# Kernel tuning notes

Measured on AMD Instinct MI355X. Metric: run time of the kernel, lower is better.

The kernel has to match this reference:

```python
import jax, jax.numpy as jnp
import numpy as np

D_MODEL = 1024
N_HEADS = 16
MAX_SEQ = 1024
BATCH = 4

def _first_primes(n):
    limit = n * 15
    sieve = np.ones(limit, dtype=bool)
    sieve[:2] = False
    for i in range(2, int(limit ** 0.5) + 1):
        if sieve[i]:
            sieve[i * i::i] = False
    return np.flatnonzero(sieve)[:n]

def _pi_attention_bias(n_heads, max_seq_len):
    # bias[h, t, s] = 0.1 * sin(prime[h]*pi * (t - s) / max_seq_len)
    primes = _first_primes(n_heads).astype(np.float32)
    freqs = primes * np.pi  # [H]
    pos = np.arange(max_seq_len, dtype=np.float32)
    pos_diff = pos[:, None] - pos[None, :]  # [T, T]
    bias = np.sin(freqs[:, None, None] * pos_diff[None] / max_seq_len) * 0.1
    return jnp.asarray(bias, dtype=jnp.float32)

def setup_inputs() -> dict:
    key = jax.random.key(0)
    ks = jax.random.split(key, 8)
    D = D_MODEL
    xavier = (6.0 / (D + D)) ** 0.5
    inp = {
        'x': jax.random.normal(ks[0], (BATCH, MAX_SEQ, D), dtype=jnp.float32),
        'Wq': jax.random.uniform(ks[1], (D, D), jnp.float32, -xavier, xavier),
        'bq': jnp.zeros((D,), jnp.float32),
        'Wk': jax.random.uniform(ks[2], (D, D), jnp.float32, -xavier, xavier),
        'bk': jnp.zeros((D,), jnp.float32),
        'Wv': jax.random.uniform(ks[3], (D, D), jnp.float32, -xavier, xavier),
        'bv': jnp.zeros((D,), jnp.float32),
        'Wo': jax.random.uniform(ks[4], (D, D), jnp.float32, -xavier, xavier),
        'bo': jnp.zeros((D,), jnp.float32),
        'pi_bias': _pi_attention_bias(N_HEADS, MAX_SEQ),
        'bias_scale': jnp.asarray(0.1, jnp.float32),
        'spectral_alpha': jnp.asarray(1.0, jnp.float32),
    }
    return inp

def reference(x, Wq, bq, Wk, bk, Wv, bv, Wo, bo, pi_bias, bias_scale, spectral_alpha):
    B, T, D = x.shape
    H = N_HEADS
    hd = D // H
    scale = 1.0 / (hd ** 0.5)

    def split_heads(y):
        return y.reshape(B, T, H, hd).transpose(0, 2, 1, 3)  # [B,H,T,hd]

    q = split_heads(x @ Wq + bq)
    k = split_heads(x @ Wk + bk)
    v = split_heads(x @ Wv + bv)

    # spectral filter along the time axis (use_spectral and T > 4)
    freqs = jnp.fft.fftfreq(T).astype(jnp.float32)  # [T]
    filt = jnp.exp(-jnp.abs(spectral_alpha) * jnp.abs(freqs))[None, None, :, None]
    q = jnp.fft.ifft(jnp.fft.fft(q, axis=2, norm='ortho') * filt, axis=2, norm='ortho').real
    k = jnp.fft.ifft(jnp.fft.fft(k, axis=2, norm='ortho') * filt, axis=2, norm='ortho').real

    scores = jnp.einsum('bhtd,bhsd->bhts', q, k) * scale
    scores = scores + bias_scale * pi_bias[None, :, :T, :T]
    attn = jax.nn.softmax(scores, axis=-1)  # dropout is identity in eval
    out = jnp.einsum('bhts,bhsd->bhtd', attn, v)
    out = out.transpose(0, 2, 1, 3).reshape(B, T, D)
    return out @ Wo + bo
```

## Files before the change

kernel.cpp:

```cpp
#include <hip/hip_runtime.h>
#include <hip/hip_bf16.h>

typedef __bf16 bf16x8 __attribute__((ext_vector_type(8)));
typedef float f32x4 __attribute__((ext_vector_type(4)));

#define OFF_GMAT   0x10000ULL
#define OFF_XB     0x210000ULL
#define OFF_XBT    0xA10000ULL
#define OFF_XF     0x1210000ULL
#define OFF_WQT    0x1A10000ULL
#define OFF_WKT    0x1C10000ULL
#define OFF_WVT    0x1E10000ULL
#define OFF_WOT    0x2010000ULL
#define OFF_KB     0x2210000ULL
#define OFF_VTB    0x2A10000ULL

static __device__ __forceinline__ unsigned short f2bf(float f) {
  union { float f; unsigned int u; } v; v.f = f;
  unsigned int r = v.u + 0x7FFFu + ((v.u >> 16) & 1u);
  return (unsigned short)(r >> 16);
}

static __device__ __forceinline__ void g2l16(const unsigned short* g, unsigned short* l) {
  __builtin_amdgcn_global_load_lds(
      (const __attribute__((address_space(1))) unsigned int*)g,
      (__attribute__((address_space(3))) unsigned int*)l, 16, 0, 0);
}

__constant__ float PRIMES_F[16] = {2.f, 3.f, 5.f, 7.f, 11.f, 13.f, 17.f, 19.f,
                                   23.f, 29.f, 31.f, 37.f, 41.f, 43.f, 47.f, 53.f};

__global__ __launch_bounds__(256) void k_prep(
    const float* __restrict__ x, const float* __restrict__ w0,
    const float* __restrict__ w1, const float* __restrict__ w2,
    const float* __restrict__ w3, const float* __restrict__ alpha_p,
    unsigned short* __restrict__ xb, unsigned short* __restrict__ xbT,
    unsigned short* __restrict__ Wout, unsigned short* __restrict__ Gm) {
  __shared__ float tile[32][33];
  const int z = blockIdx.z;
  const int r0 = blockIdx.y * 32, c0 = blockIdx.x * 32;
  const int tx = threadIdx.x & 31, ty = threadIdx.x >> 5;
  if (z == 8) {
    const float alpha = fmaxf(fabsf(alpha_p[0]), 1e-6f);
    const float q = __expf(-alpha * (1.f / 1024.f));
    const float q512 = __expf(-alpha * 0.5f);
    #pragma unroll
    for (int i = 0; i < 4; i++) {
      const int t = r0 + ty + 8 * i, s = c0 + tx;
      const int d = (t - s) & 1023;
      float s_, c_;
      __sincosf((float)d * (6.28318530717958647692f / 1024.f), &s_, &c_);
      const float sgn = (d & 1) ? -1.f : 1.f;
      const float Nr = q * c_ - q512 * sgn, Ni = q * s_;
      const float Wr = 1.f - q * c_, Wi = -q * s_;
      const float sum = (Nr * Wr + Ni * Wi) / (Wr * Wr + Wi * Wi);
      const float gd = (1.f + q512 * sgn + 2.f * sum) * (1.f / 1024.f);
      Gm[(long)t * 1024 + s] = f2bf(gd);
    }
    return;
  }
  const bool isX = z < 4;
  const float* in = isX ? (x + ((long)z << 20))
                        : (z == 4 ? w0 : z == 5 ? w1 : z == 6 ? w2 : w3);
  const long ooff = isX ? ((long)z << 20) : ((long)(z - 4) << 20);
  #pragma unroll
  for (int i = 0; i < 4; i++) {
    float v = in[(long)(r0 + ty + 8 * i) * 1024 + c0 + tx];
    tile[ty + 8 * i][tx] = v;
    if (isX) xb[ooff + (long)(r0 + ty + 8 * i) * 1024 + c0 + tx] = f2bf(v);
  }
  __syncthreads();
  unsigned short* outT = isX ? xbT : Wout;
  #pragma unroll
  for (int i = 0; i < 4; i++)
    outT[ooff + (long)(c0 + ty + 8 * i) * 1024 + r0 + tx] = f2bf(tile[tx][ty + 8 * i]);
}

#define GEMM_CORE(A_, Bt_, ACC_)                                                     \
  const int tid = threadIdx.x, l = tid & 63, wid = tid >> 6;                         \
  const int lr = l & 15, lg = l >> 4;                                                \
  const int wm = (wid >> 1) * 64, wn = (wid & 1) * 64;                               \
  const int scol = ((l & 7) ^ (l >> 3)) * 8;                                         \
  const unsigned short* Ag = A_ + (long)(m0 + wid * 32 + (l >> 3)) * 1024 + scol;    \
  const unsigned short* Bg = Bt_ + (long)(n0 + wid * 32 + (l >> 3)) * 1024 + scol;   \
  const int xk = (lr & 7) << 4;                                                      \
  const int co[2] = {(0 + lg * 16) ^ xk, (64 + lg * 16) ^ xk};                       \
  {                                                                                  \
    _Pragma("unroll")                                                                \
    for (int c = 0; c < 4; c++) {                                                    \
      g2l16(Ag + (long)c * 8192, &As[0][wid * 2048 + c * 512]);                      \
      g2l16(Bg + (long)c * 8192, &Bs[0][wid * 2048 + c * 512]);                      \
    }                                                                                \
    Ag += 64; Bg += 64;                                                              \
  }                                                                                  \
  __syncthreads();                                                                   \
  for (int t = 0; t < 16; ++t) {                                                     \
    const int cur = t & 1;                                                           \
    if (t < 15) {                                                                    \
      const int nxt = cur ^ 1;                                                       \
      _Pragma("unroll")                                                              \
      for (int c = 0; c < 4; c++) {                                                  \
        g2l16(Ag + (long)c * 8192, &As[nxt][wid * 2048 + c * 512]);                  \
        g2l16(Bg + (long)c * 8192, &Bs[nxt][wid * 2048 + c * 512]);                  \
      }                                                                              \
      Ag += 64; Bg += 64;                                                            \
      asm volatile("s_waitcnt vmcnt(8)" ::: "memory");                               \
    } else {                                                                         \
      asm volatile("s_waitcnt vmcnt(0)" ::: "memory");                               \
    }                                                                                \
    __builtin_amdgcn_s_barrier();                                                    \
    __builtin_amdgcn_sched_barrier(0);                                               \
    const char* Ab = (const char*)&As[cur][0];                                       \
    const char* Bb = (const char*)&Bs[cur][0];                                       \
    _Pragma("unroll")                                                                \
    for (int ks = 0; ks < 2; ks++) {                                                 \
      bf16x8 af[4], bfr[4];                                                          \
      _Pragma("unroll")                                                              \
      for (int mf = 0; mf < 4; mf++)                                                 \
        af[mf] = *(const bf16x8*)(Ab + (wm + mf * 16 + lr) * 128 + co[ks]);          \
      _Pragma("unroll")                                                              \
      for (int nf = 0; nf < 4; nf++)                                                 \
        bfr[nf] = *(const bf16x8*)(Bb + (wn + nf * 16 + lr) * 128 + co[ks]);         \
      _Pragma("unroll")                                                              \
      for (int mf = 0; mf < 4; mf++)                                                 \
        _Pragma("unroll")                                                            \
        for (int nf = 0; nf < 4; nf++)                                               \
          ACC_[mf][nf] = __builtin_amdgcn_mfma_f32_16x16x32_bf16(af[mf], bfr[nf],    \
                                                                 ACC_[mf][nf], 0, 0, 0); \
    }                                                                                \
    __builtin_amdgcn_sched_barrier(0);                                               \
    __builtin_amdgcn_s_barrier();                                                    \
  }

__global__ __launch_bounds__(256) void k_gemm5(
    const unsigned short* __restrict__ A, const unsigned short* __restrict__ Bt,
    const float* __restrict__ bias, const float* __restrict__ bias2,
    unsigned short* __restrict__ Cv, unsigned short* __restrict__ Cv2) {
  __shared__ __align__(16) unsigned short As[2][128 * 64];
  __shared__ __align__(16) unsigned short Bs[2][128 * 64];
  const int orig = (blockIdx.x & 7) * 64 + (blockIdx.x >> 3);
  const int m0 = (orig & 31) * 128, n0 = (orig >> 5) * 128;
  f32x4 acc[4][4] = {};
  GEMM_CORE(A, Bt, acc)
  #pragma unroll
  for (int nf = 0; nf < 4; nf++) {
    const int n = n0 + wn + nf * 16 + lr;
    const float bb = (n < 1024) ? bias[n] : bias2[n - 1024];
    unsigned short* Cd = (n < 1024) ? Cv : Cv2;
    #pragma unroll
    for (int mf = 0; mf < 4; mf++) {
      const int mb = m0 + wm + mf * 16 + lg * 4;
      #pragma unroll
      for (int r = 0; r < 4; r++)
        Cd[(long)(mb + r) * 1024 + (n & 1023)] = f2bf(acc[mf][nf][r] + bb);
    }
  }
}

__global__ __launch_bounds__(256) void k_fv(
    const unsigned short* __restrict__ Gm, const unsigned short* __restrict__ xbT,
    const unsigned short* __restrict__ WvT, const unsigned short* __restrict__ xb,
    const float* __restrict__ bv, unsigned short* __restrict__ Xf,
    unsigned short* __restrict__ Vtb) {
  __shared__ __align__(16) unsigned short As[2][128 * 64];
  __shared__ __align__(16) unsigned short Bs[2][128 * 64];
  const bool isV = blockIdx.x < 256;
  const int inner = blockIdx.x & 255;
  const int o = (inner & 7) * 32 + (inner >> 3);
  const int m0 = (o & 7) * 128, n0 = (o >> 3) * 128;
  const unsigned short* A_ = isV ? WvT : Gm;
  const unsigned short* Bt_ = isV ? xb : xbT;
  const int nk = isV ? 16 : 6;
  const int ktbase = isV ? 0 : ((m0 - 128) & 1023);
  const int tid = threadIdx.x, l = tid & 63, wid = tid >> 6;
  const int lr = l & 15, lg = l >> 4;
  const int wm = (wid >> 1) * 64, wn = (wid & 1) * 64;
  const int scol = ((l & 7) ^ (l >> 3)) * 8;
  const unsigned short* Ag = A_ + (long)(m0 + wid * 32 + (l >> 3)) * 1024 + scol;
  const unsigned short* Bg = Bt_ + (long)(n0 + wid * 32 + (l >> 3)) * 1024 + scol;
  const int xk = (lr & 7) << 4;
  const int co[2] = {(0 + lg * 16) ^ xk, (64 + lg * 16) ^ xk};
  {
    #pragma unroll
    for (int c = 0; c < 4; c++) {
      g2l16(Ag + (long)c * 8192 + ktbase, &As[0][wid * 2048 + c * 512]);
      g2l16(Bg + (long)c * 8192 + ktbase, &Bs[0][wid * 2048 + c * 512]);
    }
  }
  __syncthreads();
  f32x4 acc[4][4] = {};
  for (int t = 0; t < nk; ++t) {
    const int cur = t & 1;
    if (t < nk - 1) {
      const int nxt = cur ^ 1;
      const int kt = (ktbase + ((t + 1) << 6)) & 1023;
      #pragma unroll
      for (int c = 0; c < 4; c++) {
        g2l16(Ag + (long)c * 8192 + kt, &As[nxt][wid * 2048 + c * 512]);
        g2l16(Bg + (long)c * 8192 + kt, &Bs[nxt][wid * 2048 + c * 512]);
      }
      asm volatile("s_waitcnt vmcnt(8)" ::: "memory");
    } else {
      asm volatile("s_waitcnt vmcnt(0)" ::: "memory");
    }
    __builtin_amdgcn_s_barrier();
    __builtin_amdgcn_sched_barrier(0);
    const char* Ab = (const char*)&As[cur][0];
    const char* Bb = (const char*)&Bs[cur][0];
    #pragma unroll
    for (int ks = 0; ks < 2; ks++) {
      bf16x8 af[4], bfr[4];
      #pragma unroll
      for (int mf = 0; mf < 4; mf++)
        af[mf] = *(const bf16x8*)(Ab + (wm + mf * 16 + lr) * 128 + co[ks]);
      #pragma unroll
      for (int nf = 0; nf < 4; nf++)
        bfr[nf] = *(const bf16x8*)(Bb + (wn + nf * 16 + lr) * 128 + co[ks]);
      #pragma unroll
      for (int mf = 0; mf < 4; mf++)
        #pragma unroll
        for (int nf = 0; nf < 4; nf++)
          acc[mf][nf] = __builtin_amdgcn_mfma_f32_16x16x32_bf16(af[mf], bfr[nf], acc[mf][nf], 0, 0, 0);
    }
    __builtin_amdgcn_sched_barrier(0);
    __builtin_amdgcn_s_barrier();
  }
  #pragma unroll
  for (int nf = 0; nf < 4; nf++) {
    const int n = n0 + wn + nf * 16 + lr;
    #pragma unroll
    for (int mf = 0; mf < 4; mf++) {
      const int mb = wm + mf * 16 + lg * 4;
      #pragma unroll
      for (int r = 0; r < 4; r++) {
        const int m = m0 + mb + r;
        float v = acc[mf][nf][r];
        if (isV) {
          Vtb[(long)m * 4096 + n] = f2bf(v + bv[m]);
        } else {
          Xf[(long)((n & ~1023) + m) * 1024 + (n & 1023)] = f2bf(v);
        }
      }
    }
  }
}

__global__ __launch_bounds__(256) void k_gemmO(
    const unsigned short* __restrict__ A, const unsigned short* __restrict__ Bt,
    const float* __restrict__ bias, float* __restrict__ C) {
  __shared__ __align__(16) unsigned short As[2][64 * 64];
  __shared__ __align__(16) unsigned short Bs[2][128 * 64];
  const int orig = (blockIdx.x & 7) * 64 + (blockIdx.x >> 3);
  const int m0 = (orig & 63) * 64, n0 = (orig >> 6) * 128;
  const int tid = threadIdx.x, l = tid & 63, wid = tid >> 6;
  const int lr = l & 15, lg = l >> 4;
  const int wm = (wid >> 1) * 32, wn = (wid & 1) * 64;
  const int scol = ((l & 7) ^ (l >> 3)) * 8;
  const unsigned short* Ag = A + (long)(m0 + wid * 16 + (l >> 3)) * 1024 + scol;
  const unsigned short* Bg = Bt + (long)(n0 + wid * 32 + (l >> 3)) * 1024 + scol;
  const int xk = (lr & 7) << 4;
  const int co[2] = {(0 + lg * 16) ^ xk, (64 + lg * 16) ^ xk};
  {
    #pragma unroll
    for (int c = 0; c < 2; c++) g2l16(Ag + (long)c * 8192, &As[0][wid * 1024 + c * 512]);
    #pragma unroll
    for (int c = 0; c < 4; c++) g2l16(Bg + (long)c * 8192, &Bs[0][wid * 2048 + c * 512]);
    Ag += 64; Bg += 64;
  }
  __syncthreads();
  f32x4 acc[2][4] = {};
  for (int t = 0; t < 16; ++t) {
    const int cur = t & 1;
    if (t < 15) {
      const int nxt = cur ^ 1;
      #pragma unroll
      for (int c = 0; c < 2; c++) g2l16(Ag + (long)c * 8192, &As[nxt][wid * 1024 + c * 512]);
      #pragma unroll
      for (int c = 0; c < 4; c++) g2l16(Bg + (long)c * 8192, &Bs[nxt][wid * 2048 + c * 512]);
      Ag += 64; Bg += 64;
      asm volatile("s_waitcnt vmcnt(6)" ::: "memory");
    } else {
      asm volatile("s_waitcnt vmcnt(0)" ::: "memory");
    }
    __builtin_amdgcn_s_barrier();
    __builtin_amdgcn_sched_barrier(0);
    const char* Ab = (const char*)&As[cur][0];
    const char* Bb = (const char*)&Bs[cur][0];
    #pragma unroll
    for (int ks = 0; ks < 2; ks++) {
      bf16x8 af[2], bfr[4];
      #pragma unroll
      for (int mf = 0; mf < 2; mf++)
        af[mf] = *(const bf16x8*)(Ab + (wm + mf * 16 + lr) * 128 + co[ks]);
      #pragma unroll
      for (int nf = 0; nf < 4; nf++)
        bfr[nf] = *(const bf16x8*)(Bb + (wn + nf * 16 + lr) * 128 + co[ks]);
      #pragma unroll
      for (int mf = 0; mf < 2; mf++)
        #pragma unroll
        for (int nf = 0; nf < 4; nf++)
          acc[mf][nf] = __builtin_amdgcn_mfma_f32_16x16x32_bf16(af[mf], bfr[nf], acc[mf][nf], 0, 0, 0);
    }
    __builtin_amdgcn_sched_barrier(0);
    __builtin_amdgcn_s_barrier();
  }
  #pragma unroll
  for (int nf = 0; nf < 4; nf++) {
    const int n = n0 + wn + nf * 16 + lr;
    const float bb = bias[n];
    #pragma unroll
    for (int mf = 0; mf < 2; mf++) {
      const int mb = m0 + wm + mf * 16 + lg * 4;
      #pragma unroll
      for (int r = 0; r < 4; r++)
        C[(long)(mb + r) * 1024 + n] = acc[mf][nf][r] + bb;
    }
  }
}

__global__ __launch_bounds__(512) void k_attn(
    const unsigned short* __restrict__ Qb, const unsigned short* __restrict__ Kb,
    const unsigned short* __restrict__ Vtb,
    const float* __restrict__ bias_scale_p, unsigned short* __restrict__ Ob) {
  __shared__ __align__(16) unsigned short Kbuf[3][4096];
  __shared__ __align__(16) unsigned short Vbuf[3][4096];
  __shared__ __align__(16) unsigned short Ps[8][16 * 64];
  const int bid = blockIdx.x;
  const int qt = (bid >> 3) & 7;
  const int hb = ((bid >> 6) << 3) | (bid & 7);
  const int h = hb & 15, b = hb >> 4;
  const int tid = threadIdx.x, l = tid & 63, wid = tid >> 6;
  const int lr = l & 15, lg = l >> 4;
  const int q0 = qt * 128;
  const float LOG2E = 1.44269504088896f;
  const float c10 = bias_scale_p[0] * 0.1f * LOG2E;
  const float k1 = 0.125f * LOG2E;
  const float fh = PRIMES_F[h] * 3.14159265358979323846f;
  const unsigned short* Vth = Vtb + (long)h * 64 * 4096 + b * 1024;
  const int xk = (lr & 7) << 4;
  const int co[2] = {(0 + lg * 16) ^ xk, (64 + lg * 16) ^ xk};
  const int scol = ((l & 7) ^ (l >> 3)) * 8;

  const unsigned short* kg = Kb + (long)(b * 1024 + wid * 8 + (l >> 3)) * 1024 + h * 64 + scol;
  const unsigned short* vg = Vth + (long)(wid * 8 + (l >> 3)) * 4096 + scol;
  unsigned short* kls = &Kbuf[0][0];
  unsigned short* vls = &Vbuf[0][0];
  #define STAGE_TO(BI) \
    { g2l16(kg, kls + (BI) * 4096 + wid * 512); \
      g2l16(vg, vls + (BI) * 4096 + wid * 512); \
      kg += 64 * 1024; vg += 64; }

  STAGE_TO(0);
  STAGE_TO(1);

  bf16x8 af[2];
  #pragma unroll
  for (int ks = 0; ks < 2; ks++)
    af[ks] = *(const bf16x8*)(
        &Qb[(long)(b * 1024 + q0 + wid * 16 + lr) * 1024 + h * 64 + ks * 32 + lg * 8]);

  float st2[4], ct2[4];
  #pragma unroll
  for (int r = 0; r < 4; r++) {
    float tt = (float)(q0 + wid * 16 + lg * 4 + r);
    float s_, c_;
    __sincosf(fh * tt * (1.f / 1024.f), &s_, &c_);
    st2[r] = c10 * s_;
    ct2[r] = c10 * c_;
  }
  float ss4[4], cs4[4], sd, cd;
  __sincosf(fh * (1.f / 16.f), &sd, &cd);
  #pragma unroll
  for (int nf = 0; nf < 4; nf++)
    __sincosf(fh * (float)(nf * 16 + lr) * (1.f / 1024.f), &ss4[nf], &cs4[nf]);

  f32x4 acc_o[4] = {};
  float pden[4] = {};
  int cur = 0, stg = 2;
  __syncthreads();

  for (int it = 0; it < 16; ++it) {
    if (it < 15) {
      asm volatile("s_waitcnt vmcnt(2)" ::: "memory");
    } else {
      asm volatile("s_waitcnt vmcnt(0)" ::: "memory");
    }
    __builtin_amdgcn_s_barrier();
    __builtin_amdgcn_sched_barrier(0);
    if (it < 14) { STAGE_TO(stg); }
    const char* Kbb = (const char*)kls + cur * 8192;
    const char* Vbb = (const char*)vls + cur * 8192;
    f32x4 accs[4] = {};
    #pragma unroll
    for (int ks = 0; ks < 2; ks++) {
      bf16x8 bfr[4];
      #pragma unroll
      for (int nf = 0; nf < 4; nf++)
        bfr[nf] = *(const bf16x8*)(Kbb + (nf * 16 + lr) * 128 + co[ks]);
      __builtin_amdgcn_s_setprio(1);
      #pragma unroll
      for (int nf = 0; nf < 4; nf++)
        accs[nf] = __builtin_amdgcn_mfma_f32_16x16x32_bf16(af[ks], bfr[nf], accs[nf], 0, 0, 0);
      __builtin_amdgcn_s_setprio(0);
    }
    char* Pw = (char*)&Ps[wid][0];
    #pragma unroll
    for (int nf = 0; nf < 4; nf++) {
      #pragma unroll
      for (int r = 0; r < 4; r++) {
        float v = fmaf(accs[nf][r], k1, fmaf(st2[r], cs4[nf], -ct2[r] * ss4[nf]));
        float p;
        asm("v_exp_f32 %0, %1" : "=v"(p) : "v"(v));
        pden[r] += p;
        union { float f; unsigned int u; } pu; pu.f = p;
        const int prow = lg * 4 + r;
        *(unsigned short*)(Pw + prow * 128 + ((nf * 32 + lr * 2) ^ ((prow & 7) << 4))) =
            (unsigned short)((pu.u + 0x8000u) >> 16);
      }
    }
    #pragma unroll
    for (int ks = 0; ks < 2; ks++) {
      bf16x8 pa = *(const bf16x8*)(Pw + lr * 128 + co[ks]);
      bf16x8 vb[4];
      #pragma unroll
      for (int nf = 0; nf < 4; nf++)
        vb[nf] = *(const bf16x8*)(Vbb + (nf * 16 + lr) * 128 + co[ks]);
      __builtin_amdgcn_s_setprio(1);
      #pragma unroll
      for (int nf = 0; nf < 4; nf++)
        acc_o[nf] = __builtin_amdgcn_mfma_f32_16x16x32_bf16(pa, vb[nf], acc_o[nf], 0, 0, 0);
      __builtin_amdgcn_s_setprio(0);
    }
    #pragma unroll
    for (int nf = 0; nf < 4; nf++) {
      float c_ = cs4[nf] * cd - ss4[nf] * sd;
      ss4[nf] = ss4[nf] * cd + cs4[nf] * sd;
      cs4[nf] = c_;
    }
    cur = (cur == 2) ? 0 : cur + 1;
    stg = (stg == 2) ? 0 : stg + 1;
  }
  #undef STAGE_TO
  #pragma unroll
  for (int r = 0; r < 4; r++) {
    float dsum = pden[r];
    #pragma unroll
    for (int off = 1; off < 16; off <<= 1) dsum += __shfl_xor(dsum, off, 64);
    pden[r] = 1.0f / dsum;
  }
  const int tg = q0 + wid * 16 + lg * 4;
  #pragma unroll
  for (int nf = 0; nf < 4; nf++) {
    const int dd = nf * 16 + lr;
    #pragma unroll
    for (int r = 0; r < 4; r++) {
      float val = acc_o[nf][r] * pden[r];
      Ob[(long)(b * 1024 + tg + r) * 1024 + h * 64 + dd] = f2bf(val);
    }
  }
}

extern "C" void kernel_launch(void* const* d_in, const int* in_sizes, int n_in,
                              void* d_out, int out_size, void* d_ws, size_t ws_size,
                              hipStream_t stream) {
  const float* x   = (const float*)d_in[0];
  const float* Wq  = (const float*)d_in[1];
  const float* bq  = (const float*)d_in[2];
  const float* Wk  = (const float*)d_in[3];
  const float* bk  = (const float*)d_in[4];
  const float* Wv  = (const float*)d_in[5];
  const float* bv  = (const float*)d_in[6];
  const float* Wo  = (const float*)d_in[7];
  const float* bo  = (const float*)d_in[8];
  const float* bsc = (const float*)d_in[10];
  const float* alp = (const float*)d_in[11];
  char* ws = (char*)d_ws;
  unsigned short* Gm  = (unsigned short*)(ws + OFF_GMAT);
  unsigned short* xb  = (unsigned short*)(ws + OFF_XB);
  unsigned short* xbT = (unsigned short*)(ws + OFF_XBT);
  unsigned short* Xf  = (unsigned short*)(ws + OFF_XF);
  unsigned short* WqT = (unsigned short*)(ws + OFF_WQT);
  unsigned short* WvT = (unsigned short*)(ws + OFF_WVT);
  unsigned short* WoT = (unsigned short*)(ws + OFF_WOT);
  unsigned short* Qb  = xbT;
  unsigned short* Kb  = (unsigned short*)(ws + OFF_KB);
  unsigned short* Vtb = (unsigned short*)(ws + OFF_VTB);
  unsigned short* Ob  = Xf;

  k_prep<<<dim3(32, 32, 9), 256, 0, stream>>>(x, Wq, Wk, Wv, Wo, alp, xb, xbT, WqT, Gm);
  k_fv<<<512, 256, 0, stream>>>(Gm, xbT, WvT, xb, bv, Xf, Vtb);
  k_gemm5<<<512, 256, 0, stream>>>(Xf, WqT, bq, bk, Qb, Kb);
  k_attn<<<512, 512, 0, stream>>>(Qb, Kb, Vtb, bsc, Ob);
  k_gemmO<<<512, 256, 0, stream>>>(Ob, WoT, bo, (float*)d_out);
}
```

Baseline: 117.8 us.

## Regroup V projection with QK GEMM, single-buffer LDS, vectorize prep transpose

Moves the V projection out of the spectral-filter kernel and into the Q/K projection launch, so the filter kernel runs alone with 256 blocks and the QKV kernel runs 768 blocks. The GEMM core changes from double-buffered LDS with explicit vmcnt waits to a single buffer guarded by two __syncthreads per k-step. This halves LDS use, which may allow more resident blocks, but it gives up overlap of global loads with MFMA work. The prep transpose now uses float4 loads and ushort4 stores in place of scalar accesses.

New measurement: 119.5 us. About the same (+1.5%).

```diff
diff --git a/kernel.cpp b/kernel.cpp
--- a/kernel.cpp
+++ b/kernel.cpp
@@ -39,8 +39,8 @@
   __shared__ float tile[32][33];
   const int z = blockIdx.z;
   const int r0 = blockIdx.y * 32, c0 = blockIdx.x * 32;
-  const int tx = threadIdx.x & 31, ty = threadIdx.x >> 5;
   if (z == 8) {
+    const int tx = threadIdx.x & 31, ty = threadIdx.x >> 5;
     const float alpha = fmaxf(fabsf(alpha_p[0]), 1e-6f);
     const float q = __expf(-alpha * (1.f / 1024.f));
     const float q512 = __expf(-alpha * 0.5f);
@@ -63,20 +63,24 @@
   const float* in = isX ? (x + ((long)z << 20))
                         : (z == 4 ? w0 : z == 5 ? w1 : z == 6 ? w2 : w3);
   const long ooff = isX ? ((long)z << 20) : ((long)(z - 4) << 20);
-  #pragma unroll
-  for (int i = 0; i < 4; i++) {
-    float v = in[(long)(r0 + ty + 8 * i) * 1024 + c0 + tx];
-    tile[ty + 8 * i][tx] = v;
-    if (isX) xb[ooff + (long)(r0 + ty + 8 * i) * 1024 + c0 + tx] = f2bf(v);
-  }
+  const int ty = threadIdx.x >> 3;
+  const int c4 = (threadIdx.x & 7) * 4;
+  float4 v = *(const float4*)(in + (long)(r0 + ty) * 1024 + c0 + c4);
+  if (isX) {
+    ushort4 o; o.x = f2bf(v.x); o.y = f2bf(v.y); o.z = f2bf(v.z); o.w = f2bf(v.w);
+    *(ushort4*)(xb + ooff + (long)(r0 + ty) * 1024 + c0 + c4) = o;
+  }
+  tile[ty][c4 + 0] = v.x; tile[ty][c4 + 1] = v.y;
+  tile[ty][c4 + 2] = v.z; tile[ty][c4 + 3] = v.w;
   __syncthreads();
   unsigned short* outT = isX ? xbT : Wout;
-  #pragma unroll
-  for (int i = 0; i < 4; i++)
-    outT[ooff + (long)(c0 + ty + 8 * i) * 1024 + r0 + tx] = f2bf(tile[tx][ty + 8 * i]);
-}
-
-#define GEMM_CORE(A_, Bt_, ACC_)                                                     \
+  ushort4 o;
+  o.x = f2bf(tile[c4 + 0][ty]); o.y = f2bf(tile[c4 + 1][ty]);
+  o.z = f2bf(tile[c4 + 2][ty]); o.w = f2bf(tile[c4 + 3][ty]);
+  *(ushort4*)(outT + ooff + (long)(c0 + ty) * 1024 + r0 + c4) = o;
+}
+
+#define GEMM_CORE_SB(A_, Bt_, NK, KTOF, ACC_)                                        \
   const int tid = threadIdx.x, l = tid & 63, wid = tid >> 6;                         \
   const int lr = l & 15, lg = l >> 4;                                                \
   const int wm = (wid >> 1) * 64, wn = (wid & 1) * 64;                               \
@@ -85,33 +89,17 @@
   const unsigned short* Bg = Bt_ + (long)(n0 + wid * 32 + (l >> 3)) * 1024 + scol;   \
   const int xk = (lr & 7) << 4;                                                      \
   const int co[2] = {(0 + lg * 16) ^ xk, (64 + lg * 16) ^ xk};                       \
-  {                                                                                  \
+  for (int t = 0; t < (NK); ++t) {                                                   \
+    const int kt = KTOF(t);                                                          \
+    __syncthreads();                                                                 \
     _Pragma("unroll")                                                                \
     for (int c = 0; c < 4; c++) {                                                    \
-      g2l16(Ag + (long)c * 8192, &As[0][wid * 2048 + c * 512]);                      \
-      g2l16(Bg + (long)c * 8192, &Bs[0][wid * 2048 + c * 512]);                      \
+      g2l16(Ag + (long)c * 8192 + kt, &As[wid * 2048 + c * 512]);                    \
+      g2l16(Bg + (long)c * 8192 + kt, &Bs[wid * 2048 + c * 512]);                    \
     }                                                                                \
-    Ag += 64; Bg += 64;                                                              \
-  }                                                                                  \
-  __syncthreads();                                                                   \
-  for (int t = 0; t < 16; ++t) {                                                     \
-    const int cur = t & 1;                                                           \
-    if (t < 15) {                                                                    \
-      const int nxt = cur ^ 1;                                                       \
-      _Pragma("unroll")                                                              \
-      for (int c = 0; c < 4; c++) {                                                  \
-        g2l16(Ag + (long)c * 8192, &As[nxt][wid * 2048 + c * 512]);                  \
-        g2l16(Bg + (long)c * 8192, &Bs[nxt][wid * 2048 + c * 512]);                  \
-      }                                                                              \
-      Ag += 64; Bg += 64;                                                            \
-      asm volatile("s_waitcnt vmcnt(8)" ::: "memory");                               \
-    } else {                                                                         \
-      asm volatile("s_waitcnt vmcnt(0)" ::: "memory");                               \
-    }                                                                                \
-    __builtin_amdgcn_s_barrier();                                                    \
-    __builtin_amdgcn_sched_barrier(0);                                               \
-    const char* Ab = (const char*)&As[cur][0];                                       \
-    const char* Bb = (const char*)&Bs[cur][0];                                       \
+    __syncthreads();                                                                 \
+    const char* Ab = (const char*)&As[0];                                            \
+    const char* Bb = (const char*)&Bs[0];                                            \
     _Pragma("unroll")                                                                \
     for (int ks = 0; ks < 2; ks++) {                                                 \
       bf16x8 af[4], bfr[4];                                                          \
@@ -128,117 +116,82 @@
           ACC_[mf][nf] = __builtin_amdgcn_mfma_f32_16x16x32_bf16(af[mf], bfr[nf],    \
                                                                  ACC_[mf][nf], 0, 0, 0); \
     }                                                                                \
-    __builtin_amdgcn_sched_barrier(0);                                               \
-    __builtin_amdgcn_s_barrier();                                                    \
-  }
-
-__global__ __launch_bounds__(256) void k_gemm5(
-    const unsigned short* __restrict__ A, const unsigned short* __restrict__ Bt,
-    const float* __restrict__ bias, const float* __restrict__ bias2,
-    unsigned short* __restrict__ Cv, unsigned short* __restrict__ Cv2) {
-  __shared__ __align__(16) unsigned short As[2][128 * 64];
-  __shared__ __align__(16) unsigned short Bs[2][128 * 64];
-  const int orig = (blockIdx.x & 7) * 64 + (blockIdx.x >> 3);
-  const int m0 = (orig & 31) * 128, n0 = (orig >> 5) * 128;
+  }
+
+#define KT_LIN(t) ((t) << 6)
+
+__global__ __launch_bounds__(256) void k_fvF(
+    const unsigned short* __restrict__ Gm, const unsigned short* __restrict__ xbT,
+    unsigned short* __restrict__ Xf) {
+  __shared__ __align__(16) unsigned short As[128 * 64];
+  __shared__ __align__(16) unsigned short Bs[128 * 64];
+  const int inner = blockIdx.x;
+  const int o = (inner & 7) * 32 + (inner >> 3);
+  const int m0 = (o & 7) * 128, n0 = (o >> 3) * 128;
+  const int ktbase = (m0 - 128) & 1023;
   f32x4 acc[4][4] = {};
-  GEMM_CORE(A, Bt, acc)
+#define KT_BAND(t) ((ktbase + ((t) << 6)) & 1023)
+  GEMM_CORE_SB(Gm, xbT, 6, KT_BAND, acc)
+#undef KT_BAND
   #pragma unroll
   for (int nf = 0; nf < 4; nf++) {
     const int n = n0 + wn + nf * 16 + lr;
-    const float bb = (n < 1024) ? bias[n] : bias2[n - 1024];
-    unsigned short* Cd = (n < 1024) ? Cv : Cv2;
     #pragma unroll
     for (int mf = 0; mf < 4; mf++) {
-      const int mb = m0 + wm + mf * 16 + lg * 4;
-      #pragma unroll
-      for (int r = 0; r < 4; r++)
-        Cd[(long)(mb + r) * 1024 + (n & 1023)] = f2bf(acc[mf][nf][r] + bb);
-    }
-  }
-}
-
-__global__ __launch_bounds__(256) void k_fv(
-    const unsigned short* __restrict__ Gm, const unsigned short* __restrict__ xbT,
+      const int mb = wm + mf * 16 + lg * 4;
+      #pragma unroll
+      for (int r = 0; r < 4; r++) {
+        const int m = m0 + mb + r;
+        Xf[(long)((n & ~1023) + m) * 1024 + (n & 1023)] = f2bf(acc[mf][nf][r]);
+      }
+    }
+  }
+}
+
+__global__ __launch_bounds__(256) void k_qkv(
+    const unsigned short* __restrict__ Xf, const unsigned short* __restrict__ WqkT,
+    const float* __restrict__ bq, const float* __restrict__ bk,
+    unsigned short* __restrict__ Qb, unsigned short* __restrict__ Kb,
     const unsigned short* __restrict__ WvT, const unsigned short* __restrict__ xb,
-    const float* __restrict__ bv, unsigned short* __restrict__ Xf,
-    unsigned short* __restrict__ Vtb) {
-  __shared__ __align__(16) unsigned short As[2][128 * 64];
-  __shared__ __align__(16) unsigned short Bs[2][128 * 64];
-  const bool isV = blockIdx.x < 256;
-  const int inner = blockIdx.x & 255;
-  const int o = (inner & 7) * 32 + (inner >> 3);
-  const int m0 = (o & 7) * 128, n0 = (o >> 3) * 128;
-  const unsigned short* A_ = isV ? WvT : Gm;
-  const unsigned short* Bt_ = isV ? xb : xbT;
-  const int nk = isV ? 16 : 6;
-  const int ktbase = isV ? 0 : ((m0 - 128) & 1023);
-  const int tid = threadIdx.x, l = tid & 63, wid = tid >> 6;
-  const int lr = l & 15, lg = l >> 4;
-  const int wm = (wid >> 1) * 64, wn = (wid & 1) * 64;
-  const int scol = ((l & 7) ^ (l >> 3)) * 8;
-  const unsigned short* Ag = A_ + (long)(m0 + wid * 32 + (l >> 3)) * 1024 + scol;
-  const unsigned short* Bg = Bt_ + (long)(n0 + wid * 32 + (l >> 3)) * 1024 + scol;
-  const int xk = (lr & 7) << 4;
-  const int co[2] = {(0 + lg * 16) ^ xk, (64 + lg * 16) ^ xk};
-  {
-    #pragma unroll
-    for (int c = 0; c < 4; c++) {
-      g2l16(Ag + (long)c * 8192 + ktbase, &As[0][wid * 2048 + c * 512]);
-      g2l16(Bg + (long)c * 8192 + ktbase, &Bs[0][wid * 2048 + c * 512]);
-    }
-  }
-  __syncthreads();
+    const float* __restrict__ bv, unsigned short* __restrict__ Vtb) {
+  __shared__ __align__(16) unsigned short As[128 * 64];
+  __shared__ __align__(16) unsigned short Bs[128 * 64];
+  const int bid = blockIdx.x;
+  const bool isV = bid >= 512;
+  int m0, n0;
+  const unsigned short *A_, *Bt_;
+  if (isV) {
+    const int inner = bid - 512;
+    const int o = (inner & 7) * 32 + (inner >> 3);
+    m0 = (o & 7) * 128; n0 = (o >> 3) * 128;
+    A_ = WvT; Bt_ = xb;
+  } else {
+    const int o = (bid & 7) * 64 + (bid >> 3);
+    m0 = (o & 31) * 128; n0 = (o >> 5) * 128;
+    A_ = Xf; Bt_ = WqkT;
+  }
   f32x4 acc[4][4] = {};
-  for (int t = 0; t < nk; ++t) {
-    const int cur = t & 1;
-    if (t < nk - 1) {
-      const int nxt = cur ^ 1;
-      const int kt = (ktbase + ((t + 1) << 6)) & 1023;
-      #pragma unroll
-      for (int c = 0; c < 4; c++) {
-        g2l16(Ag + (long)c * 8192 + kt, &As[nxt][wid * 2048 + c * 512]);
-        g2l16(Bg + (long)c * 8192 + kt, &Bs[nxt][wid * 2048 + c * 512]);
-      }
-      asm volatile("s_waitcnt vmcnt(8)" ::: "memory");
-    } else {
-      asm volatile("s_waitcnt vmcnt(0)" ::: "memory");
-    }
-    __builtin_amdgcn_s_barrier();
-    __builtin_amdgcn_sched_barrier(0);
-    const char* Ab = (const char*)&As[cur][0];
-    const char* Bb = (const char*)&Bs[cur][0];
-    #pragma unroll
-    for (int ks = 0; ks < 2; ks++) {
-      bf16x8 af[4], bfr[4];
-      #pragma unroll
-      for (int mf = 0; mf < 4; mf++)
-        af[mf] = *(const bf16x8*)(Ab + (wm + mf * 16 + lr) * 128 + co[ks]);
-      #pragma unroll
-      for (int nf = 0; nf < 4; nf++)
-        bfr[nf] = *(const bf16x8*)(Bb + (wn + nf * 16 + lr) * 128 + co[ks]);
-      #pragma unroll
-      for (int mf = 0; mf < 4; mf++)
-        #pragma unroll
-        for (int nf = 0; nf < 4; nf++)
-          acc[mf][nf] = __builtin_amdgcn_mfma_f32_16x16x32_bf16(af[mf], bfr[nf], acc[mf][nf], 0, 0, 0);
-    }
-    __builtin_amdgcn_sched_barrier(0);
-    __builtin_amdgcn_s_barrier();
-  }
+  GEMM_CORE_SB(A_, Bt_, 16, KT_LIN, acc)
   #pragma unroll
   for (int nf = 0; nf < 4; nf++) {
     const int n = n0 + wn + nf * 16 + lr;
+    float bb = 0.f;
+    unsigned short* Cd = nullptr;
+    if (!isV) {
+      bb = (n < 1024) ? bq[n] : bk[n - 1024];
+      Cd = (n < 1024) ? Qb : Kb;
+    }
     #pragma unroll
     for (int mf = 0; mf < 4; mf++) {
       const int mb = wm + mf * 16 + lg * 4;
       #pragma unroll
       for (int r = 0; r < 4; r++) {
         const int m = m0 + mb + r;
-        float v = acc[mf][nf][r];
+        const float v = acc[mf][nf][r];
         if (isV) {
           Vtb[(long)m * 4096 + n] = f2bf(v + bv[m]);
         } else {
-          Xf[(long)((n & ~1023) + m) * 1024 + (n & 1023)] = f2bf(v);
+          Cd[(long)m * 1024 + (n & 1023)] = f2bf(v + bb);
         }
       }
     }
@@ -488,8 +441,8 @@
   unsigned short* Ob  = Xf;
 
   k_prep<<<dim3(32, 32, 9), 256, 0, stream>>>(x, Wq, Wk, Wv, Wo, alp, xb, xbT, WqT, Gm);
-  k_fv<<<512, 256, 0, stream>>>(Gm, xbT, WvT, xb, bv, Xf, Vtb);
-  k_gemm5<<<512, 256, 0, stream>>>(Xf, WqT, bq, bk, Qb, Kb);
+  k_fvF<<<256, 256, 0, stream>>>(Gm, xbT, Xf);
+  k_qkv<<<768, 256, 0, stream>>>(Xf, WqT, bq, bk, Qb, Kb, WvT, xb, bv, Vtb);
   k_attn<<<512, 512, 0, stream>>>(Qb, Kb, Vtb, bsc, Ob);
   k_gemmO<<<512, 256, 0, stream>>>(Ob, WoT, bo, (float*)d_out);
 }
```
